# Kernel tuning notes

Hardware: AMD Instinct MI355X
Metric: run time of the kernel (lower is better)

Reference implementation:

```python
import jax, jax.numpy as jnp
import numpy as np

N_R = 100000
N_RP1 = 200000
NNZ = 1600000
C = 128


def setup_inputs() -> dict:
    key = jax.random.key(0)
    ks = jax.random.split(key, 10)
    return {
        "x_1": jax.random.normal(ks[0], (N_R, C), dtype=jnp.float32),
        "x_2": jax.random.normal(ks[1], (N_RP1, C), dtype=jnp.float32),
        "W1": jax.random.normal(ks[2], (C, C), dtype=jnp.float32) * 0.05,
        "W2": jax.random.normal(ks[3], (C, C), dtype=jnp.float32) * 0.05,
        "vals_11": jax.random.normal(ks[4], (NNZ,), dtype=jnp.float32),
        "vals_21": jax.random.normal(ks[5], (NNZ,), dtype=jnp.float32),
        "rows_11": jax.random.randint(ks[6], (NNZ,), 0, N_R, dtype=jnp.int32),
        "cols_11": jax.random.randint(ks[7], (NNZ,), 0, N_R, dtype=jnp.int32),
        "rows_21": jax.random.randint(ks[8], (NNZ,), 0, N_R, dtype=jnp.int32),
        "cols_21": jax.random.randint(ks[9], (NNZ,), 0, N_RP1, dtype=jnp.int32),
    }


def _spmm(vals, rows, cols, x, n_out):
    # sparse [n_out, n_in] @ dense [n_in, C] via gather + segment_sum
    return jax.ops.segment_sum(vals[:, None] * x[cols], rows, num_segments=n_out)


def reference(x_1, x_2, W1, W2, vals_11, vals_21, rows_11, cols_11, rows_21, cols_21):
    n_r = x_1.shape[0]
    # Conv: x @ W, then sparse neighborhood matmul (aggr_norm=False, no update)
    x_up = jax.nn.elu(_spmm(vals_11, rows_11, cols_11, x_1 @ W1, n_r))
    x_co = jax.nn.elu(_spmm(vals_21, rows_21, cols_21, x_2 @ W2, n_r))
    return x_up + x_co
```

## Files before the change

### kernel.cpp

```cpp
#include <hip/hip_runtime.h>
#include <hip/hip_bf16.h>


#define CDIM 128
#define BIN_SHIFT 9
#define BIN_ROWS (1 << BIN_SHIFT)
#define MAX_BINS 256
#define PCHUNK 4096
#define FCAP 9216

typedef __attribute__((ext_vector_type(8))) short bf16x8;
typedef __attribute__((ext_vector_type(4))) float f32x4;

static __device__ __forceinline__ short f2bf(float f) {
  __hip_bfloat16 h = __float2bfloat16(f);
  union { __hip_bfloat16 h; short s; } u;
  u.h = h;
  return u.s;
}

__global__ __launch_bounds__(256) void hist_prep_kernel(
    const int* __restrict__ r1, const int* __restrict__ r2,
    int* __restrict__ bcnt, int nnz, int nhist,
    const float* __restrict__ W1, const float* __restrict__ W2,
    __hip_bfloat16* __restrict__ Wt1, __hip_bfloat16* __restrict__ Wt2) {
  __shared__ int c1[MAX_BINS], c2[MAX_BINS];
  int t = threadIdx.x;
  if ((int)blockIdx.x < nhist) {
    c1[t] = 0;
    c2[t] = 0;
    __syncthreads();
    int e0 = blockIdx.x * PCHUNK + t;
#pragma unroll
    for (int i = 0; i < 16; ++i) {
      int e = e0 + i * 256;
      if (e < nnz) {
        atomicAdd(&c1[r1[e] >> BIN_SHIFT], 1);
        atomicAdd(&c2[r2[e] >> BIN_SHIFT], 1);
      }
    }
    __syncthreads();
    if (c1[t]) atomicAdd(&bcnt[t], c1[t]);
    if (c2[t]) atomicAdd(&bcnt[MAX_BINS + t], c2[t]);
  } else {
    int wb = blockIdx.x - nhist;
    const float* W = wb ? W2 : W1;
    __hip_bfloat16* Wt = wb ? Wt2 : Wt1;
    for (int idx = t; idx < CDIM * CDIM; idx += 256) {
      int k = idx >> 7, n = idx & 127;
      union { __hip_bfloat16 h; short s; } u;
      u.s = f2bf(W[idx]);
      Wt[n * CDIM + k] = u.h;
    }
  }
}

__global__ __launch_bounds__(256) void scan_bins(
    const int* __restrict__ bcnt, int* __restrict__ binstart,
    int* __restrict__ bincur, int nbins, int nnz) {
  __shared__ int ws[4];
  int t = threadIdx.x, lane = t & 63, w = t >> 6;
  for (int L = 0; L < 2; ++L) {
    int v = (t < nbins) ? bcnt[L * MAX_BINS + t] : 0;
    int sc = v;
#pragma unroll
    for (int d = 1; d < 64; d <<= 1) {
      int u = __shfl_up(sc, d);
      if (lane >= d) sc += u;
    }
    if (lane == 63) ws[w] = sc;
    __syncthreads();
    int woff = 0;
    for (int i = 0; i < w; ++i) woff += ws[i];
    int excl = woff + sc - v;
    if (t < nbins) {
      binstart[L * (MAX_BINS + 1) + t] = excl;
      bincur[L * MAX_BINS + t] = excl;
    }
    if (t == 0) binstart[L * (MAX_BINS + 1) + nbins] = nnz;
    __syncthreads();
  }
}

__global__ __launch_bounds__(256) void part_gemm_kernel(
    const int* __restrict__ r1, const int* __restrict__ c1, const float* __restrict__ v1,
    const int* __restrict__ r2, const int* __restrict__ c2, const float* __restrict__ v2,
    int* __restrict__ bincur, int2* __restrict__ tmp1, int2* __restrict__ tmp2,
    int nnz, int npart,
    const float* __restrict__ x1, const __hip_bfloat16* __restrict__ Wt1,
    __hip_bfloat16* __restrict__ h1, int n_r, int ng1,
    const float* __restrict__ x2, const __hip_bfloat16* __restrict__ Wt2,
    __hip_bfloat16* __restrict__ h2, int n_rp1) {
  __shared__ int cnt[MAX_BINS], base[MAX_BINS], loff[MAX_BINS];
  int b = blockIdx.x;
  int t = threadIdx.x;

  if (b < 2 * npart) {
    int list = b >= npart;
    int pb = list ? b - npart : b;
    const int* r = list ? r2 : r1;
    const int* c = list ? c2 : c1;
    const float* v = list ? v2 : v1;
    int2* tmp = list ? tmp2 : tmp1;
    int* bcur = bincur + list * MAX_BINS;

    cnt[t] = 0;
    __syncthreads();
    int e0 = pb * PCHUNK + t;
    int rows[16];
#pragma unroll
    for (int i = 0; i < 16; ++i) {
      int e = e0 + i * 256;
      rows[i] = (e < nnz) ? r[e] : -1;
      if (rows[i] >= 0) atomicAdd(&cnt[rows[i] >> BIN_SHIFT], 1);
    }
    __syncthreads();
    {
      int n = cnt[t];
      base[t] = n ? atomicAdd(&bcur[t], n) : 0;
      loff[t] = 0;
    }
    __syncthreads();
#pragma unroll
    for (int i = 0; i < 16; ++i) {
      if (rows[i] >= 0) {
        int e = e0 + i * 256;
        int bin = rows[i] >> BIN_SHIFT;
        int o = atomicAdd(&loff[bin], 1);
        tmp[base[bin] + o] = make_int2(((rows[i] & (BIN_ROWS - 1)) << 18) | c[e],
                                       __float_as_int(v[e]));
      }
    }
    return;
  }

  b -= 2 * npart;
  const float* X;
  const __hip_bfloat16* Wt;
  __hip_bfloat16* H;
  int n_rows, bb;
  if (b < ng1) { X = x1; Wt = Wt1; H = h1; n_rows = n_r; bb = b; }
  else         { X = x2; Wt = Wt2; H = h2; n_rows = n_rp1; bb = b - ng1; }

  int lane = t & 63, wave = t >> 6;
  int rbase = bb * 128 + wave * 32;
  int lrow = lane & 15;
  int kq = (lane >> 4) * 8;

  int r0 = rbase + lrow;
  int r1r = r0 + 16;
  bool in0 = r0 < n_rows;
  bool in1 = r1r < n_rows;

  f32x4 acc0[8], acc1[8];
#pragma unroll
  for (int j = 0; j < 8; ++j) {
    acc0[j] = (f32x4){0.f, 0.f, 0.f, 0.f};
    acc1[j] = (f32x4){0.f, 0.f, 0.f, 0.f};
  }

  const float* x0p = X + (size_t)r0 * CDIM + kq;
  const float* x1p = X + (size_t)r1r * CDIM + kq;

  for (int kk = 0; kk < CDIM; kk += 32) {
    bf16x8 a0 = (bf16x8)(short)0, a1 = (bf16x8)(short)0;
    if (in0) {
      float4 u = *(const float4*)(x0p + kk);
      float4 v = *(const float4*)(x0p + kk + 4);
      a0[0] = f2bf(u.x); a0[1] = f2bf(u.y); a0[2] = f2bf(u.z); a0[3] = f2bf(u.w);
      a0[4] = f2bf(v.x); a0[5] = f2bf(v.y); a0[6] = f2bf(v.z); a0[7] = f2bf(v.w);
    }
    if (in1) {
      float4 u = *(const float4*)(x1p + kk);
      float4 v = *(const float4*)(x1p + kk + 4);
      a1[0] = f2bf(u.x); a1[1] = f2bf(u.y); a1[2] = f2bf(u.z); a1[3] = f2bf(u.w);
      a1[4] = f2bf(v.x); a1[5] = f2bf(v.y); a1[6] = f2bf(v.z); a1[7] = f2bf(v.w);
    }
    int k = kk + kq;
#pragma unroll
    for (int j = 0; j < 8; ++j) {
      int col = j * 16 + lrow;
      bf16x8 bv = *(const bf16x8*)(Wt + (size_t)col * CDIM + k);
      acc0[j] = __builtin_amdgcn_mfma_f32_16x16x32_bf16(a0, bv, acc0[j], 0, 0, 0);
      acc1[j] = __builtin_amdgcn_mfma_f32_16x16x32_bf16(a1, bv, acc1[j], 0, 0, 0);
    }
  }

  int crow = rbase + (lane >> 4) * 4;
#pragma unroll
  for (int j = 0; j < 8; ++j) {
    int col = j * 16 + lrow;
#pragma unroll
    for (int rr = 0; rr < 4; ++rr) {
      int row0 = crow + rr;
      if (row0 < n_rows) {
        union { __hip_bfloat16 h; short s; } u;
        u.s = f2bf(acc0[j][rr]);
        H[(size_t)row0 * CDIM + col] = u.h;
      }
      int row1 = crow + 16 + rr;
      if (row1 < n_rows) {
        union { __hip_bfloat16 h; short s; } u;
        u.s = f2bf(acc1[j][rr]);
        H[(size_t)row1 * CDIM + col] = u.h;
      }
    }
  }
}

__global__ __launch_bounds__(256) void fill3_kernel(
    const int2* __restrict__ tmp1, const int2* __restrict__ tmp2,
    const int* __restrict__ binstart,
    int2* __restrict__ ep1, int2* __restrict__ ep2,
    int* __restrict__ rp1, int* __restrict__ rp2,
    int n, int nnz, int nbins) {
  int L = blockIdx.y;
  const int2* tmp = L ? tmp2 : tmp1;
  int2* ep = L ? ep2 : ep1;
  int* rp = L ? rp2 : rp1;
  int bin = blockIdx.x;
  int bs = binstart[L * (MAX_BINS + 1) + bin];
  int be = binstart[L * (MAX_BINS + 1) + bin + 1];
  int count = be - bs;

  __shared__ int cnt[BIN_ROWS];
  __shared__ int wsum[4];
  __shared__ int2 outbuf[FCAP];
  int t = threadIdx.x, lane = t & 63, w = t >> 6;
  cnt[2 * t] = 0;
  cnt[2 * t + 1] = 0;
  __syncthreads();

  for (int p = bs + t; p < be; p += 256) {
    int rib = (unsigned)tmp[p].x >> 18;
    atomicAdd(&cnt[rib], 1);
  }
  __syncthreads();

  int a0 = cnt[2 * t], a1 = cnt[2 * t + 1];
  int pair = a0 + a1;
  int sc = pair;
#pragma unroll
  for (int d = 1; d < 64; d <<= 1) {
    int u = __shfl_up(sc, d);
    if (lane >= d) sc += u;
  }
  if (lane == 63) wsum[w] = sc;
  __syncthreads();
  int woff = 0;
  for (int i = 0; i < w; ++i) woff += wsum[i];
  int excl = woff + sc - pair;
  cnt[2 * t] = excl;
  cnt[2 * t + 1] = excl + a0;
  int row0 = (bin << BIN_SHIFT) + 2 * t;
  if (row0 < n) rp[row0] = bs + excl;
  if (row0 + 1 < n) rp[row0 + 1] = bs + excl + a0;
  if (bin == nbins - 1 && t == 0) rp[n] = nnz;
  __syncthreads();

  if (count <= FCAP) {
    for (int p = bs + t; p < be; p += 256) {
      int2 ev = tmp[p];
      int rib = (unsigned)ev.x >> 18;
      int slot = atomicAdd(&cnt[rib], 1);
      outbuf[slot] = make_int2(ev.x & 0x3FFFF, ev.y);
    }
    __syncthreads();
    for (int p = t; p < count; p += 256) ep[bs + p] = outbuf[p];
  } else {
    for (int p = bs + t; p < be; p += 256) {
      int2 ev = tmp[p];
      int rib = (unsigned)ev.x >> 18;
      int slot = atomicAdd(&cnt[rib], 1);
      ep[bs + slot] = make_int2(ev.x & 0x3FFFF, ev.y);
    }
  }
}

__global__ __launch_bounds__(256) void spmm_out_kernel(
    const int* __restrict__ rp1, const int2* __restrict__ ep1,
    const uint2* __restrict__ h1,
    const int* __restrict__ rp2, const int2* __restrict__ ep2,
    const uint2* __restrict__ h2,
    float* __restrict__ out, int n_r) {
  int wave = threadIdx.x >> 6;
  int lane = threadIdx.x & 63;
  int half = lane >> 5;
  int l32 = lane & 31;
  int row = blockIdx.x * 4 + wave;
  if (row >= n_r) return;

  float4 res = make_float4(0.f, 0.f, 0.f, 0.f);
#pragma unroll
  for (int L = 0; L < 2; ++L) {
    const int* rp = L ? rp2 : rp1;
    const int2* ep = L ? ep2 : ep1;
    const uint2* h = L ? h2 : h1;
    int s = rp[row], e = rp[row + 1];
    int h0n = (e - s + 1) >> 1;
    int beg = s + (half ? h0n : 0);
    int end = half ? e : s + h0n;

    float a0 = 0.f, a1 = 0.f, a2 = 0.f, a3 = 0.f;
    float b0 = 0.f, b1 = 0.f, b2 = 0.f, b3 = 0.f;
    int i = beg;
    for (; i + 1 < end; i += 2) {
      int2 ea = ep[i];
      int2 eb = ep[i + 1];
      uint2 pa = h[(size_t)(unsigned)ea.x * 32 + l32];
      uint2 pb = h[(size_t)(unsigned)eb.x * 32 + l32];
      float va = __int_as_float(ea.y);
      float vb = __int_as_float(eb.y);
      a0 += va * __uint_as_float(pa.x << 16);
      a1 += va * __uint_as_float(pa.x & 0xffff0000u);
      a2 += va * __uint_as_float(pa.y << 16);
      a3 += va * __uint_as_float(pa.y & 0xffff0000u);
      b0 += vb * __uint_as_float(pb.x << 16);
      b1 += vb * __uint_as_float(pb.x & 0xffff0000u);
      b2 += vb * __uint_as_float(pb.y << 16);
      b3 += vb * __uint_as_float(pb.y & 0xffff0000u);
    }
    if (i < end) {
      int2 ea = ep[i];
      uint2 pa = h[(size_t)(unsigned)ea.x * 32 + l32];
      float va = __int_as_float(ea.y);
      a0 += va * __uint_as_float(pa.x << 16);
      a1 += va * __uint_as_float(pa.x & 0xffff0000u);
      a2 += va * __uint_as_float(pa.y << 16);
      a3 += va * __uint_as_float(pa.y & 0xffff0000u);
    }
    float s0 = a0 + b0, s1 = a1 + b1, s2 = a2 + b2, s3 = a3 + b3;
    s0 += __shfl_xor(s0, 32);
    s1 += __shfl_xor(s1, 32);
    s2 += __shfl_xor(s2, 32);
    s3 += __shfl_xor(s3, 32);
    s0 = s0 > 0.f ? s0 : expm1f(s0);
    s1 = s1 > 0.f ? s1 : expm1f(s1);
    s2 = s2 > 0.f ? s2 : expm1f(s2);
    s3 = s3 > 0.f ? s3 : expm1f(s3);
    res.x += s0; res.y += s1; res.z += s2; res.w += s3;
  }
  if (!half) *(float4*)(out + (size_t)row * CDIM + l32 * 4) = res;
}

extern "C" void kernel_launch(void* const* d_in, const int* in_sizes, int n_in,
                              void* d_out, int out_size, void* d_ws, size_t ws_size,
                              hipStream_t stream) {
  const float* x1  = (const float*)d_in[0];
  const float* x2  = (const float*)d_in[1];
  const float* W1  = (const float*)d_in[2];
  const float* W2  = (const float*)d_in[3];
  const float* v11 = (const float*)d_in[4];
  const float* v21 = (const float*)d_in[5];
  const int* r11   = (const int*)d_in[6];
  const int* c11   = (const int*)d_in[7];
  const int* r21   = (const int*)d_in[8];
  const int* c21   = (const int*)d_in[9];

  int n_r   = in_sizes[0] / CDIM;
  int n_rp1 = in_sizes[1] / CDIM;
  int nnz   = in_sizes[4];
  float* out = (float*)d_out;
  int nbins = (n_r + BIN_ROWS - 1) >> BIN_SHIFT;

  char* ws = (char*)d_ws;
  size_t off = 0;
  auto alloc = [&](size_t bytes) -> void* {
    void* p = ws + off;
    off = (off + bytes + 255) & ~(size_t)255;
    return p;
  };
  __hip_bfloat16* h1 = (__hip_bfloat16*)alloc((size_t)n_r * CDIM * 2);
  __hip_bfloat16* h2 = (__hip_bfloat16*)alloc((size_t)n_rp1 * CDIM * 2);
  __hip_bfloat16* Wt1 = (__hip_bfloat16*)alloc(CDIM * CDIM * 2);
  __hip_bfloat16* Wt2 = (__hip_bfloat16*)alloc(CDIM * CDIM * 2);
  int* rp1  = (int*)alloc(((size_t)n_r + 1) * 4);
  int* rp2  = (int*)alloc(((size_t)n_r + 1) * 4);
  int* bcnt     = (int*)alloc(2 * MAX_BINS * 4);
  int* bincur   = (int*)alloc(2 * MAX_BINS * 4);
  int* binstart = (int*)alloc(2 * (MAX_BINS + 1) * 4);
  int2* ep1 = (int2*)alloc((size_t)nnz * 8);
  int2* ep2 = (int2*)alloc((size_t)nnz * 8);
  int2* tmp1 = (int2*)alloc((size_t)nnz * 8);
  int2* tmp2 = (int2*)alloc((size_t)nnz * 8);
  (void)ws_size;

  hipMemsetAsync(bcnt, 0, 2 * MAX_BINS * 4, stream);

  int npart = (nnz + PCHUNK - 1) / PCHUNK;
  int ng1 = (n_r + 127) / 128;
  int ng2 = (n_rp1 + 127) / 128;

  hist_prep_kernel<<<npart + 2, 256, 0, stream>>>(
      r11, r21, bcnt, nnz, npart, W1, W2, Wt1, Wt2);
  scan_bins<<<1, 256, 0, stream>>>(bcnt, binstart, bincur, nbins, nnz);

  part_gemm_kernel<<<2 * npart + ng1 + ng2, 256, 0, stream>>>(
      r11, c11, v11, r21, c21, v21, bincur, tmp1, tmp2, nnz, npart,
      x1, Wt1, h1, n_r, ng1, x2, Wt2, h2, n_rp1);

  fill3_kernel<<<dim3(nbins, 2), 256, 0, stream>>>(
      tmp1, tmp2, binstart, ep1, ep2, rp1, rp2, n_r, nnz, nbins);

  spmm_out_kernel<<<(n_r + 3) / 4, 256, 0, stream>>>(
      rp1, ep1, (const uint2*)h1,
      rp2, ep2, (const uint2*)h2, out, n_r);
}
```

Measured before the change: 322.7 us.

## Stage partitioned edges in LDS for coalesced scatter; split partition from GEMM

Partition blocks now do a local prefix scan over bin counts, write their edges sorted by bin into shared memory, then copy them out in order so each bin's run is written to global memory contiguously. This replaces scattered per-edge 8-byte stores with mostly coalesced ones. The fused partition+GEMM launch is split into two kernels, which gives the partition kernel its own LDS budget (about 40KB) but adds a launch and removes overlap between partitioning and the GEMM.

```diff
diff --git a/kernel.cpp b/kernel.cpp
--- a/kernel.cpp
+++ b/kernel.cpp
@@ -82,59 +82,87 @@
   }
 }
 
-__global__ __launch_bounds__(256) void part_gemm_kernel(
+__global__ __launch_bounds__(256) void partition_kernel(
     const int* __restrict__ r1, const int* __restrict__ c1, const float* __restrict__ v1,
     const int* __restrict__ r2, const int* __restrict__ c2, const float* __restrict__ v2,
     int* __restrict__ bincur, int2* __restrict__ tmp1, int2* __restrict__ tmp2,
-    int nnz, int npart,
+    int nnz, int npart) {
+  __shared__ int lbase[MAX_BINS];
+  __shared__ int gbase[MAX_BINS];
+  __shared__ int loff[MAX_BINS];
+  __shared__ int wsum[4];
+  __shared__ int2 sbuf[PCHUNK];
+  __shared__ unsigned char binof[PCHUNK];
+
+  int b = blockIdx.x;
+  int list = b >= npart;
+  int pb = list ? b - npart : b;
+  const int* r = list ? r2 : r1;
+  const int* c = list ? c2 : c1;
+  const float* v = list ? v2 : v1;
+  int2* tmp = list ? tmp2 : tmp1;
+  int* bcur = bincur + list * MAX_BINS;
+
+  int t = threadIdx.x, lane = t & 63, w = t >> 6;
+  lbase[t] = 0;
+  __syncthreads();
+
+  int e0 = pb * PCHUNK + t;
+  int total = nnz - pb * PCHUNK;
+  if (total > PCHUNK) total = PCHUNK;
+
+  int rows[16];
+#pragma unroll
+  for (int i = 0; i < 16; ++i) {
+    int e = e0 + i * 256;
+    rows[i] = (e < nnz) ? r[e] : -1;
+    if (rows[i] >= 0) atomicAdd(&lbase[rows[i] >> BIN_SHIFT], 1);
+  }
+  __syncthreads();
+
+  int cv = lbase[t];
+  int sc = cv;
+#pragma unroll
+  for (int d = 1; d < 64; d <<= 1) {
+    int u = __shfl_up(sc, d);
+    if (lane >= d) sc += u;
+  }
+  if (lane == 63) wsum[w] = sc;
+  __syncthreads();
+  int woff = 0;
+  for (int i = 0; i < w; ++i) woff += wsum[i];
+  int excl = woff + sc - cv;
+  lbase[t] = excl;
+  gbase[t] = cv ? atomicAdd(&bcur[t], cv) : 0;
+  loff[t] = 0;
+  __syncthreads();
+
+#pragma unroll
+  for (int i = 0; i < 16; ++i) {
+    if (rows[i] >= 0) {
+      int e = e0 + i * 256;
+      int bin = rows[i] >> BIN_SHIFT;
+      int o = atomicAdd(&loff[bin], 1);
+      int pos = lbase[bin] + o;
+      sbuf[pos] = make_int2(((rows[i] & (BIN_ROWS - 1)) << 18) | c[e],
+                            __float_as_int(v[e]));
+      binof[pos] = (unsigned char)bin;
+    }
+  }
+  __syncthreads();
+
+  for (int p = t; p < total; p += 256) {
+    int bin = binof[p];
+    tmp[gbase[bin] + (p - lbase[bin])] = sbuf[p];
+  }
+}
+
+__global__ __launch_bounds__(256) void gemm_both_kernel(
     const float* __restrict__ x1, const __hip_bfloat16* __restrict__ Wt1,
     __hip_bfloat16* __restrict__ h1, int n_r, int ng1,
     const float* __restrict__ x2, const __hip_bfloat16* __restrict__ Wt2,
     __hip_bfloat16* __restrict__ h2, int n_rp1) {
-  __shared__ int cnt[MAX_BINS], base[MAX_BINS], loff[MAX_BINS];
   int b = blockIdx.x;
-  int t = threadIdx.x;
-
-  if (b < 2 * npart) {
-    int list = b >= npart;
-    int pb = list ? b - npart : b;
-    const int* r = list ? r2 : r1;
-    const int* c = list ? c2 : c1;
-    const float* v = list ? v2 : v1;
-    int2* tmp = list ? tmp2 : tmp1;
-    int* bcur = bincur + list * MAX_BINS;
-
-    cnt[t] = 0;
-    __syncthreads();
-    int e0 = pb * PCHUNK + t;
-    int rows[16];
-#pragma unroll
-    for (int i = 0; i < 16; ++i) {
-      int e = e0 + i * 256;
-      rows[i] = (e < nnz) ? r[e] : -1;
-      if (rows[i] >= 0) atomicAdd(&cnt[rows[i] >> BIN_SHIFT], 1);
-    }
-    __syncthreads();
-    {
-      int n = cnt[t];
-      base[t] = n ? atomicAdd(&bcur[t], n) : 0;
-      loff[t] = 0;
-    }
-    __syncthreads();
-#pragma unroll
-    for (int i = 0; i < 16; ++i) {
-      if (rows[i] >= 0) {
-        int e = e0 + i * 256;
-        int bin = rows[i] >> BIN_SHIFT;
-        int o = atomicAdd(&loff[bin], 1);
-        tmp[base[bin] + o] = make_int2(((rows[i] & (BIN_ROWS - 1)) << 18) | c[e],
-                                       __float_as_int(v[e]));
-      }
-    }
-    return;
-  }
-
-  b -= 2 * npart;
   const float* X;
   const __hip_bfloat16* Wt;
   __hip_bfloat16* H;
@@ -142,6 +170,7 @@
   if (b < ng1) { X = x1; Wt = Wt1; H = h1; n_rows = n_r; bb = b; }
   else         { X = x2; Wt = Wt2; H = h2; n_rows = n_rp1; bb = b - ng1; }
 
+  int t = threadIdx.x;
   int lane = t & 63, wave = t >> 6;
   int rbase = bb * 128 + wave * 32;
   int lrow = lane & 15;
@@ -166,15 +195,15 @@
     bf16x8 a0 = (bf16x8)(short)0, a1 = (bf16x8)(short)0;
     if (in0) {
       float4 u = *(const float4*)(x0p + kk);
-      float4 v = *(const float4*)(x0p + kk + 4);
+      float4 vv = *(const float4*)(x0p + kk + 4);
       a0[0] = f2bf(u.x); a0[1] = f2bf(u.y); a0[2] = f2bf(u.z); a0[3] = f2bf(u.w);
-      a0[4] = f2bf(v.x); a0[5] = f2bf(v.y); a0[6] = f2bf(v.z); a0[7] = f2bf(v.w);
+      a0[4] = f2bf(vv.x); a0[5] = f2bf(vv.y); a0[6] = f2bf(vv.z); a0[7] = f2bf(vv.w);
     }
     if (in1) {
       float4 u = *(const float4*)(x1p + kk);
-      float4 v = *(const float4*)(x1p + kk + 4);
+      float4 vv = *(const float4*)(x1p + kk + 4);
       a1[0] = f2bf(u.x); a1[1] = f2bf(u.y); a1[2] = f2bf(u.z); a1[3] = f2bf(u.w);
-      a1[4] = f2bf(v.x); a1[5] = f2bf(v.y); a1[6] = f2bf(v.z); a1[7] = f2bf(v.w);
+      a1[4] = f2bf(vv.x); a1[5] = f2bf(vv.y); a1[6] = f2bf(vv.z); a1[7] = f2bf(vv.w);
     }
     int k = kk + kq;
 #pragma unroll
@@ -395,8 +424,10 @@
       r11, r21, bcnt, nnz, npart, W1, W2, Wt1, Wt2);
   scan_bins<<<1, 256, 0, stream>>>(bcnt, binstart, bincur, nbins, nnz);
 
-  part_gemm_kernel<<<2 * npart + ng1 + ng2, 256, 0, stream>>>(
-      r11, c11, v11, r21, c21, v21, bincur, tmp1, tmp2, nnz, npart,
+  partition_kernel<<<2 * npart, 256, 0, stream>>>(
+      r11, c11, v11, r21, c21, v21, bincur, tmp1, tmp2, nnz, npart);
+
+  gemm_both_kernel<<<ng1 + ng2, 256, 0, stream>>>(
       x1, Wt1, h1, n_r, ng1, x2, Wt2, h2, n_rp1);
 
   fill3_kernel<<<dim3(nbins, 2), 256, 0, stream>>>(
```

After: 310.0 us. 1.04x faster.
